# Performance work log

Measured on AMD Instinct MI355X. Metric: run time of the kernel, lower is better.

## Reference

```python
import jax, jax.numpy as jnp
import numpy as np

B, C, G = 2, 256, 32
SPATIAL = (16, 16, 16)
EPS = 1e-5


def setup_inputs() -> dict:
    key = jax.random.key(0)
    ks = jax.random.split(key, 11)
    s = 1.0 / np.sqrt(C)
    x = jax.random.normal(ks[0], (B, C) + SPATIAL, dtype=jnp.float32)
    mk = lambda k: jax.random.normal(k, (C, C), dtype=jnp.float32) * s
    return {
        "x": x,
        "Wq": mk(ks[1]), "bq": jnp.zeros((C,), jnp.float32),
        "Wk": mk(ks[2]), "bk": jnp.zeros((C,), jnp.float32),
        "Wv": mk(ks[3]), "bv": jnp.zeros((C,), jnp.float32),
        "Wo": mk(ks[4]), "bo": jnp.zeros((C,), jnp.float32),
        "gamma": jnp.ones((C,), jnp.float32),
        "beta": jnp.zeros((C,), jnp.float32),
    }


def reference(x, Wq, bq, Wk, bk, Wv, bv, Wo, bo, gamma, beta):
    b, c = x.shape[0], x.shape[1]
    xf = x.reshape(b, c, -1)  # [B, C, N]

    def proj1x1(inp, W, bias):
        return jnp.einsum('oc,bcn->bon', W, inp) + bias[None, :, None]

    q = proj1x1(xf, Wq, bq)
    k = proj1x1(xf, Wk, bk)
    v = proj1x1(xf, Wv, bv)

    # qk[b, n, m] = sum_c q[b, c, n] * k[b, c, m]   (no 1/sqrt(C) scale, as in source)
    scores = jnp.einsum('bcn,bcm->bnm', q, k)
    w = jax.nn.softmax(scores, axis=-1)
    # h[b, c, n] = sum_m v[b, c, m] * w[b, n, m]
    h = jnp.einsum('bcm,bnm->bcn', v, w)
    h = proj1x1(h, Wo, bo)

    y = xf + h  # residual

    # GroupNorm over (channels-in-group, spatial)
    yg = y.reshape(b, G, c // G, -1)
    mu = jnp.mean(yg, axis=(2, 3), keepdims=True)
    var = jnp.var(yg, axis=(2, 3), keepdims=True)
    yn = ((yg - mu) * jax.lax.rsqrt(var + EPS)).reshape(b, c, -1)
    yn = yn * gamma[None, :, None] + beta[None, :, None]

    out = yn * jax.nn.sigmoid(yn)  # SiLU
    return out.reshape(x.shape)
```

## Files before the change

### kernel.cpp

```cpp
#include <hip/hip_runtime.h>
#include <hip/hip_bf16.h>

typedef _Float16 f16;
typedef __attribute__((ext_vector_type(4))) _Float16 f16x4;
typedef __attribute__((ext_vector_type(8))) _Float16 f16x8;
typedef __attribute__((ext_vector_type(4))) float f32x4;

#define CD 256
#define ND 4096
#define GD 32
#define KVB 32

__device__ __forceinline__ void gl_lds16(const f16* g, f16* l) {
    __builtin_amdgcn_global_load_lds(
        (const __attribute__((address_space(1))) unsigned int*)g,
        (__attribute__((address_space(3))) unsigned int*)l,
        16, 0, 0);
}

__global__ __launch_bounds__(256)
void k_proj_qkv(const float* __restrict__ x,
                const float* __restrict__ Wq, const float* __restrict__ bq,
                const float* __restrict__ Wk, const float* __restrict__ bk,
                const float* __restrict__ Wv, const float* __restrict__ bv,
                f16* __restrict__ Qt, f16* __restrict__ Kt, f16* __restrict__ Vb)
{
    __shared__ f16 As[3][64][40];
    __shared__ f16 Bs[64][40];
    __shared__ f16 Ts[64][72];

    const int t  = threadIdx.x;
    const int n0 = blockIdx.x * 64;
    const int o0 = blockIdx.y * 64;
    const int bb = blockIdx.z;

    const float* Ws[3] = { Wq, Wk, Wv };
    const float* bs[3] = { bq, bk, bv };

    const int w  = t >> 6;
    const int l  = t & 63;
    const int lr = l & 15;
    const int lg = l >> 4;
    const int wo = (w >> 1) * 32;
    const int wn = (w & 1) * 32;

    const int sl = t & 63;
    const int k8 = (t >> 6) * 8;

    f32x4 acc[3][2][2] = {};

    for (int ck = 0; ck < CD; ck += 32) {
        __syncthreads();
#pragma unroll
        for (int p = 0; p < 3; ++p) {
            const float* s = Ws[p] + (size_t)(o0 + sl) * CD + ck + k8;
            f16x8 v;
#pragma unroll
            for (int u = 0; u < 8; ++u) v[u] = (f16)s[u];
            *(f16x8*)&As[p][sl][k8] = v;
        }
        {
            const float* s = x + ((size_t)bb * CD + ck + k8) * ND + n0 + sl;
            f16x8 v;
#pragma unroll
            for (int u = 0; u < 8; ++u) v[u] = (f16)s[(size_t)u * ND];
            *(f16x8*)&Bs[sl][k8] = v;
        }
        __syncthreads();
        f16x8 b0 = *(const f16x8*)&Bs[wn + lr][lg * 8];
        f16x8 b1 = *(const f16x8*)&Bs[wn + 16 + lr][lg * 8];
#pragma unroll
        for (int p = 0; p < 3; ++p) {
            f16x8 a0 = *(const f16x8*)&As[p][wo + lr][lg * 8];
            f16x8 a1 = *(const f16x8*)&As[p][wo + 16 + lr][lg * 8];
            acc[p][0][0] = __builtin_amdgcn_mfma_f32_16x16x32_f16(a0, b0, acc[p][0][0], 0, 0, 0);
            acc[p][0][1] = __builtin_amdgcn_mfma_f32_16x16x32_f16(a0, b1, acc[p][0][1], 0, 0, 0);
            acc[p][1][0] = __builtin_amdgcn_mfma_f32_16x16x32_f16(a1, b0, acc[p][1][0], 0, 0, 0);
            acc[p][1][1] = __builtin_amdgcn_mfma_f32_16x16x32_f16(a1, b1, acc[p][1][1], 0, 0, 0);
        }
    }

#pragma unroll
    for (int p = 0; p < 2; ++p) {
        __syncthreads();
#pragma unroll
        for (int so = 0; so < 2; ++so)
#pragma unroll
            for (int r = 0; r < 4; ++r) {
                int orow  = wo + so * 16 + lg * 4 + r;
                float bv_ = bs[p][o0 + orow];
#pragma unroll
                for (int sn = 0; sn < 2; ++sn)
                    Ts[orow][wn + sn * 16 + lr] = (f16)(acc[p][so][sn][r] + bv_);
            }
        __syncthreads();
        f16* dst = (p == 0) ? Qt : Kt;
        int n  = t >> 2;
        int o8 = (t & 3) * 16;
        f16 tmp[16];
#pragma unroll
        for (int u = 0; u < 16; ++u) tmp[u] = Ts[o8 + u][n];
        f16* g = dst + ((size_t)bb * ND + n0 + n) * CD + o0 + o8;
        *(f16x8*)g       = *(f16x8*)&tmp[0];
        *(f16x8*)(g + 8) = *(f16x8*)&tmp[8];
    }
#pragma unroll
    for (int so = 0; so < 2; ++so)
#pragma unroll
        for (int r = 0; r < 4; ++r) {
            int orow  = wo + so * 16 + lg * 4 + r;
            float bv_ = bv[o0 + orow];
#pragma unroll
            for (int sn = 0; sn < 2; ++sn) {
                int ncol = wn + sn * 16 + lr;
                Vb[((size_t)bb * CD + o0 + orow) * ND + n0 + ncol] =
                    (f16)(acc[2][so][sn][r] + bv_);
            }
        }
}

template<int KSN>
__global__ __launch_bounds__(256, 2)
void k_attn(const f16* __restrict__ Qt, const f16* __restrict__ Kt,
            const f16* __restrict__ Vb, f16* __restrict__ Op,
            float* __restrict__ ml)
{
    __shared__ f16 Ks[2][32 * 256];
    __shared__ f16 Vs[2][256 * 32];
    __shared__ f16 Pl[4][32][40];

    const int t  = threadIdx.x;
    const int w  = t >> 6;
    const int l  = t & 63;
    const int lr = l & 15;
    const int lg = l >> 4;

    const int bid = blockIdx.x;
    int bb, ks, qi;
    if constexpr (KSN == 8) {
        int xcd = bid & 7;
        bb = xcd & 1;
        ks = (xcd >> 1) | ((bid >> 8) << 2);
        qi = (bid >> 3) & 31;
    } else {
        bb = bid & 1;
        ks = (bid >> 1) & 3;
        qi = bid >> 3;
    }
    const int q0 = qi * 128 + w * 32;

    f16x8 qf[2][8];
#pragma unroll
    for (int qs = 0; qs < 2; ++qs)
#pragma unroll
        for (int kc = 0; kc < 8; ++kc)
            qf[qs][kc] = *(const f16x8*)(Qt + ((size_t)bb * ND + q0 + qs * 16 + lr) * CD + kc * 32 + lg * 8);

    f32x4 oacc[2][16] = {};
    float row_m[2] = { -3.0e38f, -3.0e38f };
    float row_l[2] = { 0.f, 0.f };

    const int kv0 = ks * (ND / KSN);
    const f16* ktb = Kt + (size_t)bb * ND * CD;
    const f16* vbb = Vb + (size_t)bb * CD * ND;

    int koff[4], voff[4];
#pragma unroll
    for (int j = 0; j < 4; ++j) {
        int v   = (w * 4 + j) * 64 + l;
        int row = v >> 5;
        int ch  = (v & 31) ^ (row & 7);
        koff[j] = row * CD + ch * 8;
        int c   = v >> 2;
        int u   = (v & 3) ^ ((c >> 1) & 3);
        voff[j] = c * ND + u * 8;
    }

    auto stage = [&](int m0, int bi) {
#pragma unroll
        for (int j = 0; j < 4; ++j)
            gl_lds16(ktb + (size_t)m0 * CD + koff[j], &Ks[bi][(w * 4 + j) * 512]);
#pragma unroll
        for (int j = 0; j < 4; ++j)
            gl_lds16(vbb + m0 + voff[j], &Vs[bi][(w * 4 + j) * 512]);
    };

    stage(kv0, 0);
    __syncthreads();

    const int NIT = (ND / KSN) / KVB;
    for (int it = 0; it < NIT; ++it) {
        const int bi = it & 1;
        if (it + 1 < NIT) stage(kv0 + (it + 1) * KVB, bi ^ 1);

        f32x4 s[2][2] = {};
        __builtin_amdgcn_s_setprio(1);
#pragma unroll
        for (int kc = 0; kc < 8; ++kc) {
            int chs = ((kc * 4 + lg) ^ (lr & 7)) * 8;
            f16x8 k0 = *(const f16x8*)&Ks[bi][(lr) * 256 + chs];
            f16x8 k1 = *(const f16x8*)&Ks[bi][(16 + lr) * 256 + chs];
            s[0][0] = __builtin_amdgcn_mfma_f32_16x16x32_f16(k0, qf[0][kc], s[0][0], 0, 0, 0);
            s[1][0] = __builtin_amdgcn_mfma_f32_16x16x32_f16(k1, qf[0][kc], s[1][0], 0, 0, 0);
            s[0][1] = __builtin_amdgcn_mfma_f32_16x16x32_f16(k0, qf[1][kc], s[0][1], 0, 0, 0);
            s[1][1] = __builtin_amdgcn_mfma_f32_16x16x32_f16(k1, qf[1][kc], s[1][1], 0, 0, 0);
        }
        __builtin_amdgcn_s_setprio(0);

#pragma unroll
        for (int qs = 0; qs < 2; ++qs) {
            float pm = fmaxf(
                fmaxf(fmaxf(s[0][qs][0], s[0][qs][1]), fmaxf(s[0][qs][2], s[0][qs][3])),
                fmaxf(fmaxf(s[1][qs][0], s[1][qs][1]), fmaxf(s[1][qs][2], s[1][qs][3])));
            pm = fmaxf(pm, __shfl_xor(pm, 16));
            pm = fmaxf(pm, __shfl_xor(pm, 32));
            bool need = (pm > row_m[qs] + 5.0f);
            float nm  = need ? pm : row_m[qs];
            float p0 = __expf(s[0][qs][0] - nm);
            float p1 = __expf(s[0][qs][1] - nm);
            float p2 = __expf(s[0][qs][2] - nm);
            float p3 = __expf(s[0][qs][3] - nm);
            float p4 = __expf(s[1][qs][0] - nm);
            float p5 = __expf(s[1][qs][1] - nm);
            float p6 = __expf(s[1][qs][2] - nm);
            float p7 = __expf(s[1][qs][3] - nm);
            float ps = ((p0 + p1) + (p2 + p3)) + ((p4 + p5) + (p6 + p7));
            ps += __shfl_xor(ps, 16);
            ps += __shfl_xor(ps, 32);
            if (__any(need)) {
                float sc = __expf(row_m[qs] - nm);
                row_l[qs] = row_l[qs] * sc + ps;
#pragma unroll
                for (int ct = 0; ct < 16; ++ct) {
                    oacc[qs][ct][0] *= sc; oacc[qs][ct][1] *= sc;
                    oacc[qs][ct][2] *= sc; oacc[qs][ct][3] *= sc;
                }
            } else {
                row_l[qs] += ps;
            }
            row_m[qs] = nm;
            f16x4 pk0 = { (f16)p0, (f16)p1, (f16)p2, (f16)p3 };
            f16x4 pk1 = { (f16)p4, (f16)p5, (f16)p6, (f16)p7 };
            *(f16x4*)&Pl[w][qs * 16 + lr][lg * 4]      = pk0;
            *(f16x4*)&Pl[w][qs * 16 + lr][16 + lg * 4] = pk1;
        }

        f16x8 pf0 = *(const f16x8*)&Pl[w][lr][lg * 8];
        f16x8 pf1 = *(const f16x8*)&Pl[w][16 + lr][lg * 8];
        __builtin_amdgcn_s_setprio(1);
#pragma unroll
        for (int ct = 0; ct < 16; ++ct) {
            f16x8 vf = *(const f16x8*)&Vs[bi][(ct * 16 + lr) * 32 + ((lg ^ ((lr >> 1) & 3))) * 8];
            oacc[0][ct] = __builtin_amdgcn_mfma_f32_16x16x32_f16(vf, pf0, oacc[0][ct], 0, 0, 0);
            oacc[1][ct] = __builtin_amdgcn_mfma_f32_16x16x32_f16(vf, pf1, oacc[1][ct], 0, 0, 0);
        }
        __builtin_amdgcn_s_setprio(0);
        __syncthreads();
    }

#pragma unroll
    for (int qs = 0; qs < 2; ++qs)
#pragma unroll
        for (int ct = 0; ct < 16; ++ct)
#pragma unroll
            for (int r = 0; r < 4; ++r) {
                int cch = ct * 16 + lg * 4 + r;
                Op[(((size_t)ks * 2 + bb) * CD + cch) * ND + q0 + qs * 16 + lr] =
                    (f16)oacc[qs][ct][r];
            }
    if (lg == 0) {
#pragma unroll
        for (int qs = 0; qs < 2; ++qs) {
            int n = q0 + qs * 16 + lr;
            ml[((ks * 2 + bb) * 2 + 0) * ND + n] = row_m[qs];
            ml[((ks * 2 + bb) * 2 + 1) * ND + n] = row_l[qs];
        }
    }
}

template<int KSN>
__global__ __launch_bounds__(256)
void k_ml(const float* __restrict__ ml, float* __restrict__ wq)
{
    int i = blockIdx.x * 256 + threadIdx.x;
    int b = i / ND, n = i % ND;
    float m[KSN], lv[KSN];
#pragma unroll
    for (int ks = 0; ks < KSN; ++ks) {
        m[ks]  = ml[((ks * 2 + b) * 2 + 0) * ND + n];
        lv[ks] = ml[((ks * 2 + b) * 2 + 1) * ND + n];
    }
    float M = m[0];
#pragma unroll
    for (int ks = 1; ks < KSN; ++ks) M = fmaxf(M, m[ks]);
    float wgt[KSN], L = 0.f;
#pragma unroll
    for (int ks = 0; ks < KSN; ++ks) { wgt[ks] = __expf(m[ks] - M); L += wgt[ks] * lv[ks]; }
    float inv = 1.0f / L;
#pragma unroll
    for (int ks = 0; ks < KSN; ++ks)
        wq[(ks * 2 + b) * ND + n] = wgt[ks] * inv;
}

template<int KSN>
__global__ __launch_bounds__(256)
void k_comb(const f16* __restrict__ Op, const float* __restrict__ wq,
            f16* __restrict__ Hb)
{
    size_t i = (size_t)blockIdx.x * 256 + threadIdx.x;
    int n0 = (int)(i % (ND / 8)) * 8;
    int c  = (int)((i / (ND / 8)) % CD);
    int b  = (int)(i / ((size_t)CD * (ND / 8)));

    float acc[8] = {};
#pragma unroll
    for (int ks = 0; ks < KSN; ++ks) {
        f16x8 o = *(const f16x8*)(Op + (((size_t)ks * 2 + b) * CD + c) * ND + n0);
        const float* wp = wq + (ks * 2 + b) * ND + n0;
        float4 w0 = *(const float4*)wp;
        float4 w1 = *(const float4*)(wp + 4);
        acc[0] += w0.x * (float)o[0]; acc[1] += w0.y * (float)o[1];
        acc[2] += w0.z * (float)o[2]; acc[3] += w0.w * (float)o[3];
        acc[4] += w1.x * (float)o[4]; acc[5] += w1.y * (float)o[5];
        acc[6] += w1.z * (float)o[6]; acc[7] += w1.w * (float)o[7];
    }
    f16x8 h;
#pragma unroll
    for (int u = 0; u < 8; ++u) h[u] = (f16)acc[u];
    *(f16x8*)(Hb + ((size_t)b * CD + c) * ND + n0) = h;
}

__global__ __launch_bounds__(256)
void k_proj_o(const f16* __restrict__ Hb, const float* __restrict__ Wo,
              const float* __restrict__ bo, const float* __restrict__ x,
              float* __restrict__ Y)
{
    __shared__ f16 As[64][40];
    __shared__ f16 Bs[64][40];

    const int t  = threadIdx.x;
    const int n0 = blockIdx.x * 64;
    const int o0 = blockIdx.y * 64;
    const int bb = blockIdx.z;

    const int w  = t >> 6;
    const int l  = t & 63;
    const int lr = l & 15;
    const int lg = l >> 4;
    const int wo = (w >> 1) * 32;
    const int wn = (w & 1) * 32;

    const int sl = t & 63;
    const int k8 = (t >> 6) * 8;

    f32x4 acc[2][2] = {};

    for (int ck = 0; ck < CD; ck += 32) {
        __syncthreads();
        {
            const float* s = Wo + (size_t)(o0 + sl) * CD + ck + k8;
            f16x8 v;
#pragma unroll
            for (int u = 0; u < 8; ++u) v[u] = (f16)s[u];
            *(f16x8*)&As[sl][k8] = v;
        }
        {
            const f16* s = Hb + ((size_t)bb * CD + ck + k8) * ND + n0 + sl;
            f16x8 v;
#pragma unroll
            for (int u = 0; u < 8; ++u) v[u] = s[(size_t)u * ND];
            *(f16x8*)&Bs[sl][k8] = v;
        }
        __syncthreads();
        f16x8 a0 = *(const f16x8*)&As[wo + lr][lg * 8];
        f16x8 a1 = *(const f16x8*)&As[wo + 16 + lr][lg * 8];
        f16x8 b0 = *(const f16x8*)&Bs[wn + lr][lg * 8];
        f16x8 b1 = *(const f16x8*)&Bs[wn + 16 + lr][lg * 8];
        acc[0][0] = __builtin_amdgcn_mfma_f32_16x16x32_f16(a0, b0, acc[0][0], 0, 0, 0);
        acc[0][1] = __builtin_amdgcn_mfma_f32_16x16x32_f16(a0, b1, acc[0][1], 0, 0, 0);
        acc[1][0] = __builtin_amdgcn_mfma_f32_16x16x32_f16(a1, b0, acc[1][0], 0, 0, 0);
        acc[1][1] = __builtin_amdgcn_mfma_f32_16x16x32_f16(a1, b1, acc[1][1], 0, 0, 0);
    }

#pragma unroll
    for (int so = 0; so < 2; ++so)
#pragma unroll
        for (int r = 0; r < 4; ++r) {
            int orow  = wo + so * 16 + lg * 4 + r;
            float bv_ = bo[o0 + orow];
#pragma unroll
            for (int sn = 0; sn < 2; ++sn) {
                int ncol   = wn + sn * 16 + lr;
                size_t idx = ((size_t)bb * CD + o0 + orow) * ND + n0 + ncol;
                Y[idx] = acc[so][sn][r] + bv_ + x[idx];
            }
        }
}

__global__ __launch_bounds__(256)
void k_gn_silu(const float* __restrict__ Y, const float* __restrict__ gamma,
               const float* __restrict__ beta, float* __restrict__ out)
{
    const int g = blockIdx.x, b = blockIdx.y;
    const size_t base = ((size_t)b * CD + g * 8) * ND;
    const float4* src = (const float4*)(Y + base);

    float s = 0.f, s2 = 0.f;
    for (int i = threadIdx.x; i < (8 * ND) / 4; i += 256) {
        float4 v = src[i];
        s  += v.x + v.y + v.z + v.w;
        s2 += v.x * v.x + v.y * v.y + v.z * v.z + v.w * v.w;
    }
#pragma unroll
    for (int m = 1; m < 64; m <<= 1) {
        s  += __shfl_xor(s, m);
        s2 += __shfl_xor(s2, m);
    }
    __shared__ float red[8];
    __shared__ float mr[2];
    if ((threadIdx.x & 63) == 0) {
        red[(threadIdx.x >> 6) * 2]     = s;
        red[(threadIdx.x >> 6) * 2 + 1] = s2;
    }
    __syncthreads();
    if (threadIdx.x == 0) {
        float S  = red[0] + red[2] + red[4] + red[6];
        float S2 = red[1] + red[3] + red[5] + red[7];
        float mean = S / 32768.f;
        float var  = S2 / 32768.f - mean * mean;
        mr[0] = mean;
        mr[1] = rsqrtf(var + 1e-5f);
    }
    __syncthreads();
    const float mean = mr[0], rstd = mr[1];

    float4* dst = (float4*)(out + base);
    for (int i = threadIdx.x; i < (8 * ND) / 4; i += 256) {
        int c = g * 8 + (i >> 10);
        float ga = gamma[c], be = beta[c];
        float4 v = src[i];
        float in[4] = { v.x, v.y, v.z, v.w };
        float ob[4];
#pragma unroll
        for (int u = 0; u < 4; ++u) {
            float yn = (in[u] - mean) * rstd * ga + be;
            float sg = 1.0f / (1.0f + __expf(-yn));
            ob[u] = yn * sg;
        }
        dst[i] = *(float4*)ob;
    }
}

extern "C" void kernel_launch(void* const* d_in, const int* in_sizes, int n_in,
                              void* d_out, int out_size, void* d_ws, size_t ws_size,
                              hipStream_t stream)
{
    const float* x     = (const float*)d_in[0];
    const float* Wq    = (const float*)d_in[1];
    const float* bq    = (const float*)d_in[2];
    const float* Wk    = (const float*)d_in[3];
    const float* bk    = (const float*)d_in[4];
    const float* Wv    = (const float*)d_in[5];
    const float* bv    = (const float*)d_in[6];
    const float* Wo    = (const float*)d_in[7];
    const float* bo    = (const float*)d_in[8];
    const float* gamma = (const float*)d_in[9];
    const float* beta  = (const float*)d_in[10];

    char* ws = (char*)d_ws;
    f16* Qt = (f16*)(ws);
    f16* Kt = (f16*)(ws + (4u << 20));
    f16* Vb = (f16*)(ws + (8u << 20));
    f16* Hb = (f16*)(ws + (12u << 20));
    f16* Op = (f16*)(ws + (16u << 20));
    float* Y = (float*)(ws + (16u << 20));

    const bool big = ws_size >= (50ull << 20);

    k_proj_qkv<<<dim3(64, 4, 2), 256, 0, stream>>>(x, Wq, bq, Wk, bk, Wv, bv, Qt, Kt, Vb);

    if (big) {
        constexpr int KSN = 8;
        float* ml    = (float*)(ws + (48u << 20));
        float* wq    = (float*)(ws + (48u << 20) + (768u << 10));
        k_attn<KSN><<<dim3(32 * KSN * 2), 256, 0, stream>>>(Qt, Kt, Vb, Op, ml);
        k_ml<KSN><<<dim3((2 * ND) / 256), 256, 0, stream>>>(ml, wq);
        k_comb<KSN><<<dim3((2 * CD * ND / 8) / 256), 256, 0, stream>>>(Op, wq, Hb);
        k_proj_o<<<dim3(64, 4, 2), 256, 0, stream>>>(Hb, Wo, bo, x, Y);
        k_gn_silu<<<dim3(GD, 2), 256, 0, stream>>>(Y, gamma, beta, (float*)d_out);
    } else {
        constexpr int KSN = 4;
        float* ml    = (float*)(ws + (32u << 20));
        float* wq    = (float*)(ws + (32u << 20) + (512u << 10));
        k_attn<KSN><<<dim3(32 * KSN * 2), 256, 0, stream>>>(Qt, Kt, Vb, Op, ml);
        k_ml<KSN><<<dim3((2 * ND) / 256), 256, 0, stream>>>(ml, wq);
        k_comb<KSN><<<dim3((2 * CD * ND / 8) / 256), 256, 0, stream>>>(Op, wq, Hb);
        k_proj_o<<<dim3(64, 4, 2), 256, 0, stream>>>(Hb, Wo, bo, x, Y);
        k_gn_silu<<<dim3(GD, 2), 256, 0, stream>>>(Y, gamma, beta, (float*)d_out);
    }
}
```

Measured before the change: 121.2 us.

## Fuse GroupNorm statistics into output projection epilogue and widen GN grid

```diff
diff --git a/kernel.cpp b/kernel.cpp
--- a/kernel.cpp
+++ b/kernel.cpp
@@ -189,6 +189,7 @@
     __syncthreads();
 
     const int NIT = (ND / KSN) / KVB;
+#pragma unroll 2
     for (int it = 0; it < NIT; ++it) {
         const int bi = it & 1;
         if (it + 1 < NIT) stage(kv0 + (it + 1) * KVB, bi ^ 1);
@@ -333,10 +334,11 @@
 __global__ __launch_bounds__(256)
 void k_proj_o(const f16* __restrict__ Hb, const float* __restrict__ Wo,
               const float* __restrict__ bo, const float* __restrict__ x,
-              float* __restrict__ Y)
+              float* __restrict__ Y, float* __restrict__ part)
 {
     __shared__ f16 As[64][40];
     __shared__ f16 Bs[64][40];
+    __shared__ float rs[4][2][2][2];
 
     const int t  = threadIdx.x;
     const int n0 = blockIdx.x * 64;
@@ -383,7 +385,8 @@
     }
 
 #pragma unroll
-    for (int so = 0; so < 2; ++so)
+    for (int so = 0; so < 2; ++so) {
+        float ls = 0.f, ls2 = 0.f;
 #pragma unroll
         for (int r = 0; r < 4; ++r) {
             int orow  = wo + so * 16 + lg * 4 + r;
@@ -392,53 +395,69 @@
             for (int sn = 0; sn < 2; ++sn) {
                 int ncol   = wn + sn * 16 + lr;
                 size_t idx = ((size_t)bb * CD + o0 + orow) * ND + n0 + ncol;
-                Y[idx] = acc[so][sn][r] + bv_ + x[idx];
+                float v = acc[so][sn][r] + bv_ + x[idx];
+                Y[idx] = v;
+                ls  += v;
+                ls2 += v * v;
             }
         }
+#pragma unroll
+        for (int m = 1; m <= 16; m <<= 1) {
+            ls  += __shfl_xor(ls, m);
+            ls2 += __shfl_xor(ls2, m);
+        }
+        if ((l & 31) == 0) {
+            rs[w][so][l >> 5][0] = ls;
+            rs[w][so][l >> 5][1] = ls2;
+        }
+    }
+    __syncthreads();
+    if (t < 16) {
+        int gl = t >> 1, st = t & 1;
+        int a = gl >> 2, so = (gl >> 1) & 1, lh = gl & 1;
+        float v = rs[2 * a][so][lh][st] + rs[2 * a + 1][so][lh][st];
+        part[(((size_t)bb * GD + (o0 >> 3) + gl) * 64 + blockIdx.x) * 2 + st] = v;
+    }
 }
 
 __global__ __launch_bounds__(256)
-void k_gn_silu(const float* __restrict__ Y, const float* __restrict__ gamma,
-               const float* __restrict__ beta, float* __restrict__ out)
-{
-    const int g = blockIdx.x, b = blockIdx.y;
+void k_gn_silu(const float* __restrict__ Y, const float* __restrict__ part,
+               const float* __restrict__ gamma, const float* __restrict__ beta,
+               float* __restrict__ out)
+{
+    const int g  = blockIdx.x, b = blockIdx.y, nq = blockIdx.z;
+    const int t  = threadIdx.x;
+
+    __shared__ float mr[2];
+    if (t < 64) {
+        float s  = part[(((size_t)b * GD + g) * 64 + t) * 2 + 0];
+        float s2 = part[(((size_t)b * GD + g) * 64 + t) * 2 + 1];
+#pragma unroll
+        for (int m = 1; m < 64; m <<= 1) {
+            s  += __shfl_xor(s, m);
+            s2 += __shfl_xor(s2, m);
+        }
+        if (t == 0) {
+            float mean = s / 32768.f;
+            float var  = s2 / 32768.f - mean * mean;
+            mr[0] = mean;
+            mr[1] = rsqrtf(var + 1e-5f);
+        }
+    }
+    __syncthreads();
+    const float mean = mr[0], rstd = mr[1];
+
     const size_t base = ((size_t)b * CD + g * 8) * ND;
     const float4* src = (const float4*)(Y + base);
-
-    float s = 0.f, s2 = 0.f;
-    for (int i = threadIdx.x; i < (8 * ND) / 4; i += 256) {
-        float4 v = src[i];
-        s  += v.x + v.y + v.z + v.w;
-        s2 += v.x * v.x + v.y * v.y + v.z * v.z + v.w * v.w;
-    }
-#pragma unroll
-    for (int m = 1; m < 64; m <<= 1) {
-        s  += __shfl_xor(s, m);
-        s2 += __shfl_xor(s2, m);
-    }
-    __shared__ float red[8];
-    __shared__ float mr[2];
-    if ((threadIdx.x & 63) == 0) {
-        red[(threadIdx.x >> 6) * 2]     = s;
-        red[(threadIdx.x >> 6) * 2 + 1] = s2;
-    }
-    __syncthreads();
-    if (threadIdx.x == 0) {
-        float S  = red[0] + red[2] + red[4] + red[6];
-        float S2 = red[1] + red[3] + red[5] + red[7];
-        float mean = S / 32768.f;
-        float var  = S2 / 32768.f - mean * mean;
-        mr[0] = mean;
-        mr[1] = rsqrtf(var + 1e-5f);
-    }
-    __syncthreads();
-    const float mean = mr[0], rstd = mr[1];
-
     float4* dst = (float4*)(out + base);
-    for (int i = threadIdx.x; i < (8 * ND) / 4; i += 256) {
-        int c = g * 8 + (i >> 10);
+
+    for (int i = t; i < 2048; i += 256) {
+        int ch = i >> 8;
+        int nn = i & 255;
+        int f4 = ch * (ND / 4) + nq * 256 + nn;
+        int c  = g * 8 + ch;
         float ga = gamma[c], be = beta[c];
-        float4 v = src[i];
+        float4 v = src[f4];
         float in[4] = { v.x, v.y, v.z, v.w };
         float ob[4];
 #pragma unroll
@@ -447,7 +466,7 @@
             float sg = 1.0f / (1.0f + __expf(-yn));
             ob[u] = yn * sg;
         }
-        dst[i] = *(float4*)ob;
+        dst[f4] = *(float4*)ob;
     }
 }
 
@@ -481,21 +500,23 @@
 
     if (big) {
         constexpr int KSN = 8;
-        float* ml    = (float*)(ws + (48u << 20));
-        float* wq    = (float*)(ws + (48u << 20) + (768u << 10));
+        float* ml   = (float*)(ws + (48u << 20));
+        float* wq   = (float*)(ws + (48u << 20) + (768u << 10));
+        float* part = (float*)(ws + (49u << 20) + (512u << 10));
         k_attn<KSN><<<dim3(32 * KSN * 2), 256, 0, stream>>>(Qt, Kt, Vb, Op, ml);
         k_ml<KSN><<<dim3((2 * ND) / 256), 256, 0, stream>>>(ml, wq);
         k_comb<KSN><<<dim3((2 * CD * ND / 8) / 256), 256, 0, stream>>>(Op, wq, Hb);
-        k_proj_o<<<dim3(64, 4, 2), 256, 0, stream>>>(Hb, Wo, bo, x, Y);
-        k_gn_silu<<<dim3(GD, 2), 256, 0, stream>>>(Y, gamma, beta, (float*)d_out);
+        k_proj_o<<<dim3(64, 4, 2), 256, 0, stream>>>(Hb, Wo, bo, x, Y, part);
+        k_gn_silu<<<dim3(GD, 2, 4), 256, 0, stream>>>(Y, part, gamma, beta, (float*)d_out);
     } else {
         constexpr int KSN = 4;
-        float* ml    = (float*)(ws + (32u << 20));
-        float* wq    = (float*)(ws + (32u << 20) + (512u << 10));
+        float* ml   = (float*)(ws + (32u << 20));
+        float* wq   = (float*)(ws + (32u << 20) + (512u << 10));
+        float* part = (float*)(ws + (33u << 20));
         k_attn<KSN><<<dim3(32 * KSN * 2), 256, 0, stream>>>(Qt, Kt, Vb, Op, ml);
         k_ml<KSN><<<dim3((2 * ND) / 256), 256, 0, stream>>>(ml, wq);
         k_comb<KSN><<<dim3((2 * CD * ND / 8) / 256), 256, 0, stream>>>(Op, wq, Hb);
-        k_proj_o<<<dim3(64, 4, 2), 256, 0, stream>>>(Hb, Wo, bo, x, Y);
-        k_gn_silu<<<dim3(GD, 2), 256, 0, stream>>>(Y, gamma, beta, (float*)d_out);
-    }
-}
+        k_proj_o<<<dim3(64, 4, 2), 256, 0, stream>>>(Hb, Wo, bo, x, Y, part);
+        k_gn_silu<<<dim3(GD, 2, 4), 256, 0, stream>>>(Y, part, gamma, beta, (float*)d_out);
+    }
+}
```

Measured after the change: 117.7 us. 2.9% less time.
